# Performance work log

Measured on AMD Instinct MI355X. Metric: run time of the kernel, lower is better.

## Reference

```python
import jax, jax.numpy as jnp
import numpy as np

U, E, V = 1024, 256, 20200

def _w(key, shape):
    fan_in = shape[0] if len(shape) > 1 else shape[0]
    return jax.random.normal(key, shape, dtype=jnp.float32) * (1.0 / np.sqrt(fan_in))

def setup_inputs() -> dict:
    key = jax.random.key(0)
    ks = jax.random.split(key, 20)
    inp = {
        'enc_in': jax.random.randint(ks[0], (32, 64), 0, V),
        'teacher': jax.random.randint(ks[1], (32, 16), 0, V),
        'max_cmd_len': 16,
        'batch_size': 32,
        # encoder params
        'Ee': jax.random.normal(ks[2], (V, E), dtype=jnp.float32) * 0.02,
        'enc_Wx': _w(ks[3], (E, 3 * U)),
        'enc_Wh': _w(ks[4], (U, 3 * U)),
        'enc_b_in': jnp.zeros((3 * U,), jnp.float32),
        'enc_b_rec': jnp.zeros((3 * U,), jnp.float32),
        # decoder params
        'Ed': jax.random.normal(ks[5], (V, E), dtype=jnp.float32) * 0.02,
        'dec_Wx': _w(ks[6], (U + E, 3 * U)),
        'dec_Wh': _w(ks[7], (U, 3 * U)),
        'dec_b_in': jnp.zeros((3 * U,), jnp.float32),
        'dec_b_rec': jnp.zeros((3 * U,), jnp.float32),
        # Bahdanau attention params
        'W1': _w(ks[8], (U, U)), 'b1': jnp.zeros((U,), jnp.float32),
        'W2': _w(ks[9], (U, U)), 'b2': jnp.zeros((U,), jnp.float32),
        'Va': _w(ks[10], (U, 1)), 'bv': jnp.zeros((1,), jnp.float32),
        # output projection
        'Wf': _w(ks[11], (U, V)), 'bf': jnp.zeros((V,), jnp.float32),
    }
    return inp

def gru_step(x, h, Wx, Wh, b_in, b_rec):
    # Keras GRU, reset_after=True, gate order (z, r, h)
    gx = x @ Wx + b_in          # [B, 3U]
    gh = h @ Wh + b_rec         # [B, 3U]
    xz, xr, xh = jnp.split(gx, 3, axis=-1)
    hz, hr, hh = jnp.split(gh, 3, axis=-1)
    z = jax.nn.sigmoid(xz + hz)
    r = jax.nn.sigmoid(xr + hr)
    c = jnp.tanh(xh + r * hh)
    return z * h + (1.0 - z) * c

def reference(enc_in, teacher, max_cmd_len, batch_size,
              Ee, enc_Wx, enc_Wh, enc_b_in, enc_b_rec,
              Ed, dec_Wx, dec_Wh, dec_b_in, dec_b_rec,
              W1, b1, W2, b2, Va, bv, Wf, bf):
    B = enc_in.shape[0]
    # ----- encoder: GRU over source, h0 = 0 -----
    x_emb = Ee[enc_in]                          # [B, S, E]
    def enc_step(h, x_t):
        h_new = gru_step(x_t, h, enc_Wx, enc_Wh, enc_b_in, enc_b_rec)
        return h_new, h_new
    enc_hidden, enc_seq = jax.lax.scan(enc_step, jnp.zeros((B, U), x_emb.dtype),
                                       jnp.swapaxes(x_emb, 0, 1))
    encoded = jnp.swapaxes(enc_seq, 0, 1)       # [B, S, U]

    # ----- decoder: teacher-forced, attention each step -----
    pre_enc = encoded @ W1 + b1                 # precompute W1(encoded): [B, S, U]
    h0_dec = jnp.zeros((B, U), encoded.dtype)   # original calls gru without initial_state

    def dec_step(dec_h, tok):
        q = dec_h @ W2 + b2                                     # [B, U]
        score = jnp.tanh(pre_enc + q[:, None, :]) @ Va + bv     # [B, S, 1]
        attn = jax.nn.softmax(score, axis=1)
        ctx = jnp.sum(attn * encoded, axis=1)                   # [B, U]
        x = jnp.concatenate([ctx, Ed[tok]], axis=-1)            # [B, U+E]
        h_new = gru_step(x, h0_dec, dec_Wx, dec_Wh, dec_b_in, dec_b_rec)
        logits_t = h_new @ Wf + bf                              # [B, V]
        return h_new, logits_t

    toks = jnp.swapaxes(teacher[:, :max_cmd_len], 0, 1)         # [T, B]
    _, logits_tbv = jax.lax.scan(dec_step, enc_hidden, toks)    # [T, B, V]
    logits = jnp.swapaxes(logits_tbv, 0, 1)                     # [B, T, V]
    predictions = jnp.argmax(logits, axis=-1).astype(jnp.int64) # [B, T]
    return logits, predictions
```

## Files before the change

kernel.cpp:

```cpp
#include <hip/hip_runtime.h>
#include <cmath>

#define BB 32
#define SS 64
#define TT 16
#define UU 1024
#define EE 256
#define VV 20200
#define G3 3072
#define NBLK 256

#define WS_XEMBT 0
#define WS_HT    (WS_XEMBT + SS*EE*BB)
#define WS_ENC   (WS_HT + 2*UU*BB)
#define WS_PRE   (WS_ENC + BB*SS*UU)
#define WS_Q     (WS_PRE + BB*SS*UU)
#define WS_ESC   (WS_Q + BB*UU)
#define WS_XT    (WS_ESC + BB*SS)
#define WS_HDT   (WS_XT + UU*BB)
#define WS_HD    (WS_HDT + UU*BB)
#define WS_DEMB  (WS_HD + BB*TT*UU)
#define WS_GXD   (WS_DEMB + BB*TT*EE)
#define WS_BAR   (WS_GXD + BB*TT*G3)

#define ACC4(A, V, S) do { (A).x += (V).x * (S); (A).y += (V).y * (S); \
                           (A).z += (V).z * (S); (A).w += (V).w * (S); } while (0)
#define RED4(A, M) do { (A).x += __shfl_xor((A).x, M, 64); (A).y += __shfl_xor((A).y, M, 64); \
                        (A).z += __shfl_xor((A).z, M, 64); (A).w += __shfl_xor((A).w, M, 64); } while (0)

__device__ __forceinline__ float sigmoidf_(float x) {
    return 1.0f / (1.0f + expf(-x));
}

__device__ __forceinline__ void store_agent(float* p, float v) {
    __hip_atomic_store(p, v, __ATOMIC_RELAXED, __HIP_MEMORY_SCOPE_AGENT);
}
__device__ __forceinline__ void store_agent_u(unsigned* p, unsigned v) {
    __hip_atomic_store(p, v, __ATOMIC_RELAXED, __HIP_MEMORY_SCOPE_AGENT);
}
__device__ __forceinline__ unsigned load_agent_u(unsigned* p) {
    return __hip_atomic_load(p, __ATOMIC_RELAXED, __HIP_MEMORY_SCOPE_AGENT);
}

__device__ __forceinline__ void grid_barrier(unsigned* base, int bid, unsigned g) {
    __syncthreads();
    if (threadIdx.x < 64) {
        const int lane = threadIdx.x;
        const int grp = bid >> 5;
        const unsigned gv = g + 1u;
        if (lane == 0) {
            __builtin_amdgcn_s_waitcnt(0);
            store_agent_u(base + bid, gv);
        }
        if ((bid & 31) == 0) {
            for (;;) {
                unsigned v = load_agent_u(base + grp * 32 + (lane & 31));
                if (__all((int)(v >= gv))) break;
                __builtin_amdgcn_s_sleep(2);
            }
            if (lane == 0) store_agent_u(base + 256 + grp * 32, gv);
            if (bid == 0) {
                for (;;) {
                    unsigned v = load_agent_u(base + 256 + (lane & 7) * 32);
                    if (__all((int)(v >= gv))) break;
                    __builtin_amdgcn_s_sleep(2);
                }
                if (lane < 8) store_agent_u(base + 512 + lane * 32, gv);
            }
        }
        if (bid != 0) {
            while (load_agent_u(base + 512 + grp * 32) < gv) {
                __builtin_amdgcn_s_sleep(2);
            }
        }
        __builtin_amdgcn_fence(__ATOMIC_ACQUIRE, "agent");
    }
    __syncthreads();
}

__global__ __launch_bounds__(256) void k_prep(const int* __restrict__ enc_in,
                                              const float* __restrict__ Ee,
                                              const int* __restrict__ teacher,
                                              const float* __restrict__ Ed,
                                              float* __restrict__ ws) {
    int gid = blockIdx.x * 256 + threadIdx.x;
    const int NE = SS * EE * BB;
    const int NH = UU * BB;
    const int ND = BB * TT * EE;
    if (gid < NE) {
        int b = gid & 31;
        int e = (gid >> 5) & 255;
        int s = gid >> 13;
        ws[WS_XEMBT + gid] = Ee[(size_t)enc_in[b * SS + s] * EE + e];
    } else if (gid < NE + NH) {
        ws[WS_HT + (gid - NE)] = 0.0f;
    } else if (gid < NE + NH + ND) {
        int idx = gid - NE - NH;
        int e = idx & 255;
        int row = idx >> 8;
        int t = row >> 5, b = row & 31;
        ws[WS_DEMB + idx] = Ed[(size_t)teacher[b * TT + t] * EE + e];
    } else if (gid < NE + NH + ND + 3072) {
        ((unsigned*)(ws + WS_BAR))[gid - NE - NH - ND] = 0u;
    }
}

__global__ __launch_bounds__(512, 2) void k_encoder(const float* __restrict__ Wh,
                                                    const float* __restrict__ Wx,
                                                    const float* __restrict__ b_in,
                                                    const float* __restrict__ b_rec,
                                                    float* __restrict__ ws) {
    float* XembT = ws + WS_XEMBT;
    float* hT = ws + WS_HT;
    float* enc = ws + WS_ENC;
    unsigned* bar = (unsigned*)(ws + WS_BAR);

    __shared__ float Whs[12288];
    __shared__ float Wxs[3072];
    __shared__ float scr[4096];

    const int tid = threadIdx.x;
    const int bid = blockIdx.x;
    const int wv = tid >> 6;
    const int lane = tid & 63;
    const int kp = lane & 7;
    const int rg = lane >> 3;

    for (int k = tid; k < 1024; k += 512) {
        #pragma unroll
        for (int g = 0; g < 3; ++g)
            *(float4*)(Whs + k * 12 + g * 4) =
                *(const float4*)(Wh + (size_t)k * G3 + g * 1024 + bid * 4);
    }
    if (tid < 256) {
        int k = tid;
        #pragma unroll
        for (int g = 0; g < 3; ++g)
            *(float4*)(Wxs + k * 12 + g * 4) =
                *(const float4*)(Wx + (size_t)k * G3 + g * 1024 + bid * 4);
    }

    float bz_s = 0.f, br_s = 0.f, bci_s = 0.f, bcr_s = 0.f;
    int rc_ = 0, rb_ = 0, rj_ = 0;
    if (tid < 128) {
        rc_ = tid >> 5; rb_ = tid & 31; rj_ = bid * 4 + rc_;
        bz_s = b_in[rj_] + b_rec[rj_];
        br_s = b_in[1024 + rj_] + b_rec[1024 + rj_];
        bci_s = b_in[2048 + rj_];
        bcr_s = b_rec[2048 + rj_];
    }
    __syncthreads();

    const int hk0 = wv * 128 + kp;
    const int xk0 = wv * 32 + kp;
    float hreg = 0.f;

    for (int t = 0; t < SS; ++t) {
        const float* hprev = hT + (t & 1) * (UU * BB);
        float* hnext = hT + ((t & 1) ^ 1) * (UU * BB);

        float4 az[4], ar[4], ah[4], ax[4];
        #pragma unroll
        for (int c = 0; c < 4; ++c) {
            az[c] = make_float4(0.f, 0.f, 0.f, 0.f);
            ar[c] = make_float4(0.f, 0.f, 0.f, 0.f);
            ah[c] = make_float4(0.f, 0.f, 0.f, 0.f);
            ax[c] = make_float4(0.f, 0.f, 0.f, 0.f);
        }

        {
            const float* hp = hprev + hk0 * 32 + rg * 4;
            float4 hb[16];
            #pragma unroll
            for (int u = 0; u < 16; ++u) hb[u] = *(const float4*)(hp + u * 256);
            #pragma unroll
            for (int u = 0; u < 16; ++u) {
                const float* wp = Whs + (hk0 + 8 * u) * 12;
                float4 wz = *(const float4*)wp;
                float4 wr_ = *(const float4*)(wp + 4);
                float4 wc_ = *(const float4*)(wp + 8);
                float4 hv = hb[u];
                ACC4(az[0], hv, wz.x); ACC4(az[1], hv, wz.y); ACC4(az[2], hv, wz.z); ACC4(az[3], hv, wz.w);
                ACC4(ar[0], hv, wr_.x); ACC4(ar[1], hv, wr_.y); ACC4(ar[2], hv, wr_.z); ACC4(ar[3], hv, wr_.w);
                ACC4(ah[0], hv, wc_.x); ACC4(ah[1], hv, wc_.y); ACC4(ah[2], hv, wc_.z); ACC4(ah[3], hv, wc_.w);
            }
        }
        {
            const float* xp = XembT + t * (EE * BB) + xk0 * 32 + rg * 4;
            float4 xb[4];
            #pragma unroll
            for (int u = 0; u < 4; ++u) xb[u] = *(const float4*)(xp + u * 256);
            #pragma unroll
            for (int u = 0; u < 4; ++u) {
                const float* wp = Wxs + (xk0 + 8 * u) * 12;
                float4 wz = *(const float4*)wp;
                float4 wr_ = *(const float4*)(wp + 4);
                float4 wc_ = *(const float4*)(wp + 8);
                float4 xv = xb[u];
                ACC4(az[0], xv, wz.x); ACC4(az[1], xv, wz.y); ACC4(az[2], xv, wz.z); ACC4(az[3], xv, wz.w);
                ACC4(ar[0], xv, wr_.x); ACC4(ar[1], xv, wr_.y); ACC4(ar[2], xv, wr_.z); ACC4(ar[3], xv, wr_.w);
                ACC4(ax[0], xv, wz.x * 0.f + wc_.x); ACC4(ax[1], xv, wc_.y); ACC4(ax[2], xv, wc_.z); ACC4(ax[3], xv, wc_.w);
            }
        }
        #pragma unroll
        for (int m = 1; m <= 4; m <<= 1) {
            #pragma unroll
            for (int c = 0; c < 4; ++c) { RED4(az[c], m); RED4(ar[c], m); RED4(ah[c], m); RED4(ax[c], m); }
        }
        if (kp == 0) {
            float* sb = scr + wv * 512 + rg * 4;
            #pragma unroll
            for (int c = 0; c < 4; ++c) {
                *(float4*)(sb + c * 32) = az[c];
                *(float4*)(sb + 128 + c * 32) = ar[c];
                *(float4*)(sb + 256 + c * 32) = ah[c];
                *(float4*)(sb + 384 + c * 32) = ax[c];
            }
        }
        __syncthreads();
        if (tid < 128) {
            float saz = 0.f, sar = 0.f, sah = 0.f, sax = 0.f;
            #pragma unroll
            for (int w = 0; w < 8; ++w) {
                const float* sb = scr + w * 512 + rc_ * 32 + rb_;
                saz += sb[0]; sar += sb[128]; sah += sb[256]; sax += sb[384];
            }
            float z = sigmoidf_(saz + bz_s);
            float r = sigmoidf_(sar + br_s);
            float cc = tanhf(sax + bci_s + r * (sah + bcr_s));
            float hnew = z * hreg + (1.0f - z) * cc;
            hreg = hnew;
            store_agent(&hnext[rj_ * 32 + rb_], hnew);
            enc[((size_t)rb_ * SS + t) * UU + rj_] = hnew;
        }
        grid_barrier(bar, bid, (unsigned)t);
    }
}

__global__ __launch_bounds__(256) void k_gemm(const float* __restrict__ A,
                                              const float* __restrict__ Bm,
                                              const float* __restrict__ bias,
                                              float* __restrict__ C,
                                              int M, int N, int K) {
    __shared__ float As[16][68];
    __shared__ float Bs[16][132];
    const int rb = blockIdx.x * 64;
    const int cb = blockIdx.y * 128;
    const int tid = threadIdx.x;
    const int cg = tid & 31;
    const int rg = tid >> 5;
    float acc[8][4] = {{0.f}};

    const int arow = tid >> 2, akq = (tid & 3) * 4;
    const int bkk = tid >> 4, bc8 = (tid & 15) * 8;
    const bool nfull = (cb + 128 <= N);

    for (int k0 = 0; k0 < K; k0 += 16) {
        {
            float4 a4 = *(const float4*)(A + (size_t)(rb + arow) * K + k0 + akq);
            As[akq + 0][arow] = a4.x; As[akq + 1][arow] = a4.y;
            As[akq + 2][arow] = a4.z; As[akq + 3][arow] = a4.w;
        }
        {
            int col = cb + bc8;
            const float* bp = Bm + (size_t)(k0 + bkk) * N + col;
            if (nfull) {
                float4 x0 = *(const float4*)bp;
                float4 x1 = *(const float4*)(bp + 4);
                Bs[bkk][bc8 + 0] = x0.x; Bs[bkk][bc8 + 1] = x0.y; Bs[bkk][bc8 + 2] = x0.z; Bs[bkk][bc8 + 3] = x0.w;
                Bs[bkk][bc8 + 4] = x1.x; Bs[bkk][bc8 + 5] = x1.y; Bs[bkk][bc8 + 6] = x1.z; Bs[bkk][bc8 + 7] = x1.w;
            } else {
                #pragma unroll
                for (int jj = 0; jj < 8; ++jj)
                    Bs[bkk][bc8 + jj] = (col + jj < N) ? bp[jj] : 0.0f;
            }
        }
        __syncthreads();
        #pragma unroll
        for (int kk = 0; kk < 16; ++kk) {
            float4 a0 = *(const float4*)&As[kk][rg * 8];
            float4 a1 = *(const float4*)&As[kk][rg * 8 + 4];
            float4 b0 = *(const float4*)&Bs[kk][cg * 4];
            float av[8] = {a0.x, a0.y, a0.z, a0.w, a1.x, a1.y, a1.z, a1.w};
            float bv[4] = {b0.x, b0.y, b0.z, b0.w};
            #pragma unroll
            for (int i = 0; i < 8; ++i)
                #pragma unroll
                for (int jj = 0; jj < 4; ++jj)
                    acc[i][jj] += av[i] * bv[jj];
        }
        __syncthreads();
    }
    const int col0 = cb + cg * 4;
    const bool cfull = (col0 + 4 <= N);
    #pragma unroll
    for (int i = 0; i < 8; ++i) {
        int row = rb + rg * 8 + i;
        float* cp = C + (size_t)row * N + col0;
        if (cfull) {
            float4 o;
            o.x = acc[i][0] + bias[col0 + 0];
            o.y = acc[i][1] + bias[col0 + 1];
            o.z = acc[i][2] + bias[col0 + 2];
            o.w = acc[i][3] + bias[col0 + 3];
            *(float4*)cp = o;
        } else {
            #pragma unroll
            for (int jj = 0; jj < 4; ++jj)
                if (col0 + jj < N) cp[jj] = acc[i][jj] + bias[col0 + jj];
        }
    }
}

__global__ __launch_bounds__(256) void k_gemm128(const float* __restrict__ A,
                                                 const float* __restrict__ Bm,
                                                 const float* __restrict__ bias,
                                                 float* __restrict__ C,
                                                 int M, int N, int K) {
    __shared__ float As[16][132];
    __shared__ float Bs[16][132];
    const int rb = blockIdx.x * 128;
    const int cb = blockIdx.y * 128;
    const int tid = threadIdx.x;
    const int rg = tid >> 4;
    const int cg = tid & 15;
    float acc[8][8] = {{0.f}};

    const int arow = tid >> 1, akq = (tid & 1) * 8;
    const int bkk = tid >> 4, bc8 = (tid & 15) * 8;
    const bool nfull = (cb + 128 <= N);

    for (int k0 = 0; k0 < K; k0 += 16) {
        {
            const float* ap = A + (size_t)(rb + arow) * K + k0 + akq;
            float4 a0 = *(const float4*)ap;
            float4 a1 = *(const float4*)(ap + 4);
            As[akq + 0][arow] = a0.x; As[akq + 1][arow] = a0.y;
            As[akq + 2][arow] = a0.z; As[akq + 3][arow] = a0.w;
            As[akq + 4][arow] = a1.x; As[akq + 5][arow] = a1.y;
            As[akq + 6][arow] = a1.z; As[akq + 7][arow] = a1.w;
        }
        {
            int col = cb + bc8;
            const float* bp = Bm + (size_t)(k0 + bkk) * N + col;
            if (nfull) {
                *(float4*)&Bs[bkk][bc8] = *(const float4*)bp;
                *(float4*)&Bs[bkk][bc8 + 4] = *(const float4*)(bp + 4);
            } else {
                #pragma unroll
                for (int jj = 0; jj < 8; ++jj)
                    Bs[bkk][bc8 + jj] = (col + jj < N) ? bp[jj] : 0.0f;
            }
        }
        __syncthreads();
        #pragma unroll
        for (int kk = 0; kk < 16; ++kk) {
            float4 a0 = *(const float4*)&As[kk][rg * 8];
            float4 a1 = *(const float4*)&As[kk][rg * 8 + 4];
            float4 b0 = *(const float4*)&Bs[kk][cg * 8];
            float4 b1 = *(const float4*)&Bs[kk][cg * 8 + 4];
            float av[8] = {a0.x, a0.y, a0.z, a0.w, a1.x, a1.y, a1.z, a1.w};
            float bw[8] = {b0.x, b0.y, b0.z, b0.w, b1.x, b1.y, b1.z, b1.w};
            #pragma unroll
            for (int i = 0; i < 8; ++i)
                #pragma unroll
                for (int jj = 0; jj < 8; ++jj)
                    acc[i][jj] += av[i] * bw[jj];
        }
        __syncthreads();
    }
    const int col0 = cb + cg * 8;
    const bool cfull = (col0 + 8 <= N);
    #pragma unroll
    for (int i = 0; i < 8; ++i) {
        int row = rb + rg * 8 + i;
        float* cp = C + (size_t)row * N + col0;
        if (cfull) {
            float4 o0, o1;
            o0.x = acc[i][0] + bias[col0 + 0];
            o0.y = acc[i][1] + bias[col0 + 1];
            o0.z = acc[i][2] + bias[col0 + 2];
            o0.w = acc[i][3] + bias[col0 + 3];
            o1.x = acc[i][4] + bias[col0 + 4];
            o1.y = acc[i][5] + bias[col0 + 5];
            o1.z = acc[i][6] + bias[col0 + 6];
            o1.w = acc[i][7] + bias[col0 + 7];
            *(float4*)cp = o0;
            *(float4*)(cp + 4) = o1;
        } else {
            #pragma unroll
            for (int jj = 0; jj < 8; ++jj)
                if (col0 + jj < N) cp[jj] = acc[i][jj] + bias[col0 + jj];
        }
    }
}

__global__ __launch_bounds__(256, 1) void k_decoder(const float* __restrict__ W2,
                                                    const float* __restrict__ b2,
                                                    const float* __restrict__ Va,
                                                    const float* __restrict__ bv,
                                                    const float* __restrict__ Wxd,
                                                    const float* __restrict__ b_rec,
                                                    float* __restrict__ ws) {
    float* hT = ws + WS_HT;
    float* enc = ws + WS_ENC;
    float* pre = ws + WS_PRE;
    float* q = ws + WS_Q;
    float* esc = ws + WS_ESC;
    float* xT = ws + WS_XT;
    float* hdT = ws + WS_HDT;
    float* Hd = ws + WS_HD;
    float* GXd = ws + WS_GXD;
    unsigned* bar = (unsigned*)(ws + WS_BAR) + 1024;

    __shared__ float Wxds[12288];
    __shared__ float W2s[4096];
    __shared__ float scr[1536];
    __shared__ float eL[64];
    __shared__ float attnL[64];
    __shared__ float shs[256];

    const int tid = threadIdx.x;
    const int bid = blockIdx.x;
    const int wv = tid >> 6;
    const int lane = tid & 63;
    const int kp = lane & 7;
    const int rg = lane >> 3;

    for (int k = tid; k < 1024; k += 256) {
        #pragma unroll
        for (int g = 0; g < 3; ++g)
            *(float4*)(Wxds + k * 12 + g * 4) =
                *(const float4*)(Wxd + (size_t)k * G3 + g * 1024 + bid * 4);
        *(float4*)(W2s + k * 4) = *(const float4*)(W2 + (size_t)k * UU + bid * 4);
    }

    float bzr_s = 0.f, brr_s = 0.f, bcr_s = 0.f;
    int rc_ = 0, rb_ = 0, rj_ = 0;
    if (tid < 128) {
        rc_ = tid >> 5; rb_ = tid & 31; rj_ = bid * 4 + rc_;
        bzr_s = b_rec[rj_];
        brr_s = b_rec[1024 + rj_];
        bcr_s = b_rec[2048 + rj_];
    }
    __syncthreads();

    const int xk0 = wv * 256 + kp;
    unsigned bc = 0;

    for (int t = 0; t < TT; ++t) {
        const float* hsrc = (t == 0) ? hT : hdT;

        float gxz = 0.f, gxr = 0.f, gxc = 0.f;
        if (tid < 128) {
            const float* gx = GXd + (size_t)(t * BB + rb_) * G3;
            gxz = gx[rj_];
            gxr = gx[1024 + rj_];
            gxc = gx[2048 + rj_];
        }

        {
            const int cq = lane & 3;
            const int kpq = (lane >> 2) & 7;
            const int rgq = (lane >> 5) | (wv << 1);
            const int qc = bid * 4 + cq;
            const float* hp = hsrc + kpq * 32 + rgq * 4;
            float a0 = 0, a1 = 0, a2 = 0, a3 = 0;
            for (int g = 0; g < 16; ++g) {
                float4 hv[8]; float wr[8];
                #pragma unroll
                for (int u = 0; u < 8; ++u) {
                    hv[u] = *(const float4*)(hp + (g * 8 + u) * 256);
                    wr[u] = W2s[(kpq + 8 * (g * 8 + u)) * 4 + cq];
                }
                #pragma unroll
                for (int u = 0; u < 8; ++u) {
                    a0 += hv[u].x * wr[u]; a1 += hv[u].y * wr[u];
                    a2 += hv[u].z * wr[u]; a3 += hv[u].w * wr[u];
                }
            }
            #pragma unroll
            for (int m = 4; m <= 16; m <<= 1) {
                a0 += __shfl_xor(a0, m, 64); a1 += __shfl_xor(a1, m, 64);
                a2 += __shfl_xor(a2, m, 64); a3 += __shfl_xor(a3, m, 64);
            }
            if (kpq == 0) {
                float bb2 = b2[qc];
                store_agent(&q[(size_t)(rgq * 4 + 0) * UU + qc], a0 + bb2);
                store_agent(&q[(size_t)(rgq * 4 + 1) * UU + qc], a1 + bb2);
                store_agent(&q[(size_t)(rgq * 4 + 2) * UU + qc], a2 + bb2);
                store_agent(&q[(size_t)(rgq * 4 + 3) * UU + qc], a3 + bb2);
            }
        }
        grid_barrier(bar, bid, bc++);

        {
            const int b = bid >> 3, s0 = (bid & 7) * 8;
            const int pi = tid >> 5, kq = tid & 31;
            const int srow = s0 + pi;
            const float* pe = pre + ((size_t)b * SS + srow) * UU;
            const float* qb = q + (size_t)b * UU;
            float acc = 0;
            #pragma unroll
            for (int kk = 0; kk < 8; ++kk) {
                int k = kq * 32 + kk * 4;
                float4 p4 = *(const float4*)(pe + k);
                float4 q4 = *(const float4*)(qb + k);
                float4 v4 = *(const float4*)(Va + k);
                acc += tanhf(p4.x + q4.x) * v4.x + tanhf(p4.y + q4.y) * v4.y +
                       tanhf(p4.z + q4.z) * v4.z + tanhf(p4.w + q4.w) * v4.w;
            }
            #pragma unroll
            for (int m = 16; m >= 1; m >>= 1) acc += __shfl_xor(acc, m, 32);
            if (kq == 0) store_agent(&esc[b * SS + srow], acc + bv[0]);
        }
        grid_barrier(bar, bid, bc++);

        {
            const int b = bid >> 3, ug = bid & 7;
            if (tid < 64) eL[tid] = esc[b * SS + tid];
            __syncthreads();
            if (tid < 64) {
                float v = eL[tid];
                float m = v;
                #pragma unroll
                for (int mm = 32; mm >= 1; mm >>= 1) m = fmaxf(m, __shfl_xor(m, mm, 64));
                float p = expf(v - m);
                float sum = p;
                #pragma unroll
                for (int mm = 32; mm >= 1; mm >>= 1) sum += __shfl_xor(sum, mm, 64);
                attnL[tid] = p / sum;
            }
            __syncthreads();
            const int u = ug * 128 + (tid & 127), sp = tid >> 7;
            float acc = 0;
            #pragma unroll 8
            for (int i = 0; i < 32; ++i) {
                int srow = sp * 32 + i;
                acc += attnL[srow] * enc[((size_t)b * SS + srow) * UU + u];
            }
            shs[(tid & 127) * 2 + sp] = acc;
            __syncthreads();
            if (tid < 128)
                store_agent(&xT[(size_t)(ug * 128 + tid) * BB + b], shs[tid * 2] + shs[tid * 2 + 1]);
        }
        grid_barrier(bar, bid, bc++);

        {
            float4 sz[4], sr_[4], sc_[4];
            #pragma unroll
            for (int c = 0; c < 4; ++c) {
                sz[c] = make_float4(0.f, 0.f, 0.f, 0.f);
                sr_[c] = make_float4(0.f, 0.f, 0.f, 0.f);
                sc_[c] = make_float4(0.f, 0.f, 0.f, 0.f);
            }
            const float* xp = xT + xk0 * 32 + rg * 4;
            #pragma unroll
            for (int gg = 0; gg < 2; ++gg) {
                float4 xb[16];
                #pragma unroll
                for (int u = 0; u < 16; ++u) xb[u] = *(const float4*)(xp + (gg * 16 + u) * 256);
                #pragma unroll
                for (int u = 0; u < 16; ++u) {
                    const float* wp = Wxds + (xk0 + 8 * (gg * 16 + u)) * 12;
                    float4 wz = *(const float4*)wp;
                    float4 wr4 = *(const float4*)(wp + 4);
                    float4 wc4 = *(const float4*)(wp + 8);
                    float4 xv = xb[u];
                    ACC4(sz[0], xv, wz.x); ACC4(sz[1], xv, wz.y); ACC4(sz[2], xv, wz.z); ACC4(sz[3], xv, wz.w);
                    ACC4(sr_[0], xv, wr4.x); ACC4(sr_[1], xv, wr4.y); ACC4(sr_[2], xv, wr4.z); ACC4(sr_[3], xv, wr4.w);
                    ACC4(sc_[0], xv, wc4.x); ACC4(sc_[1], xv, wc4.y); ACC4(sc_[2], xv, wc4.z); ACC4(sc_[3], xv, wc4.w);
                }
            }
            #pragma unroll
            for (int m = 1; m <= 4; m <<= 1) {
                #pragma unroll
                for (int c = 0; c < 4; ++c) { RED4(sz[c], m); RED4(sr_[c], m); RED4(sc_[c], m); }
            }
            if (kp == 0) {
                float* sb = scr + wv * 384 + rg * 4;
                #pragma unroll
                for (int c = 0; c < 4; ++c) {
                    *(float4*)(sb + c * 32) = sz[c];
                    *(float4*)(sb + 128 + c * 32) = sr_[c];
                    *(float4*)(sb + 256 + c * 32) = sc_[c];
                }
            }
            __syncthreads();
            if (tid < 128) {
                float ssz = 0.f, ssr = 0.f, ssc = 0.f;
                #pragma unroll
                for (int w = 0; w < 4; ++w) {
                    const float* sb = scr + w * 384 + rc_ * 32 + rb_;
                    ssz += sb[0]; ssr += sb[128]; ssc += sb[256];
                }
                float z = sigmoidf_(ssz + gxz + bzr_s);
                float rr = sigmoidf_(ssr + gxr + brr_s);
                float cc = tanhf(ssc + gxc + rr * bcr_s);
                float h = (1.0f - z) * cc;
                Hd[((size_t)rb_ * TT + t) * UU + rj_] = h;
                store_agent(&hdT[(size_t)rj_ * BB + rb_], h);
            }
        }
        grid_barrier(bar, bid, bc++);
    }
}

__global__ __launch_bounds__(256) void k_argmax(const float* __restrict__ logits,
                                                float* __restrict__ outp) {
    const int row = blockIdx.x;
    const float* lr = logits + (size_t)row * VV;
    const int tid = threadIdx.x;
    float best = -INFINITY;
    int bidx = 0x7fffffff;
    for (int c = tid; c < VV; c += 256) {
        float v = lr[c];
        if (v > best) { best = v; bidx = c; }
    }
    __shared__ float bv_[256];
    __shared__ int bi_[256];
    bv_[tid] = best; bi_[tid] = bidx;
    __syncthreads();
    for (int s2 = 128; s2 > 0; s2 >>= 1) {
        if (tid < s2) {
            float ov = bv_[tid + s2]; int oi = bi_[tid + s2];
            if (ov > bv_[tid] || (ov == bv_[tid] && oi < bi_[tid])) {
                bv_[tid] = ov; bi_[tid] = oi;
            }
        }
        __syncthreads();
    }
    if (tid == 0) outp[row] = (float)bi_[0];
}

extern "C" void kernel_launch(void* const* d_in, const int* in_sizes, int n_in,
                              void* d_out, int out_size, void* d_ws, size_t ws_size,
                              hipStream_t stream) {
    const int* enc_in = (const int*)d_in[0];
    const int* teacher = (const int*)d_in[1];
    const float* Ee = (const float*)d_in[4];
    const float* eWx = (const float*)d_in[5];
    const float* eWh = (const float*)d_in[6];
    const float* eb_in = (const float*)d_in[7];
    const float* eb_rec = (const float*)d_in[8];
    const float* Ed = (const float*)d_in[9];
    const float* dWx = (const float*)d_in[10];
    const float* db_in = (const float*)d_in[12];
    const float* db_rec = (const float*)d_in[13];
    const float* W1 = (const float*)d_in[14];
    const float* b1 = (const float*)d_in[15];
    const float* W2 = (const float*)d_in[16];
    const float* b2 = (const float*)d_in[17];
    const float* Va = (const float*)d_in[18];
    const float* bvv = (const float*)d_in[19];
    const float* Wf = (const float*)d_in[20];
    const float* bf = (const float*)d_in[21];
    float* ws = (float*)d_ws;
    float* out = (float*)d_out;

    const int NTOT = SS * EE * BB + UU * BB + BB * TT * EE + 3072;
    k_prep<<<dim3((NTOT + 255) / 256), dim3(256), 0, stream>>>(enc_in, Ee, teacher, Ed, ws);

    k_gemm<<<dim3(8, 24), dim3(256), 0, stream>>>(ws + WS_DEMB, dWx + (size_t)UU * G3, db_in,
                                                  ws + WS_GXD, BB * TT, G3, EE);

    k_encoder<<<dim3(NBLK), dim3(512), 0, stream>>>(eWh, eWx, eb_in, eb_rec, ws);

    k_gemm<<<dim3(32, 8), dim3(256), 0, stream>>>(ws + WS_ENC, W1, b1, ws + WS_PRE, BB * SS, UU, UU);

    k_decoder<<<dim3(NBLK), dim3(256), 0, stream>>>(W2, b2, Va, bvv, dWx, db_rec, ws);

    k_gemm128<<<dim3(4, 158), dim3(256), 0, stream>>>(ws + WS_HD, Wf, bf, out, BB * TT, VV, UU);

    k_argmax<<<dim3(BB * TT), dim3(256), 0, stream>>>(out, out + (size_t)BB * TT * VV);
}
```

Measured before the change: 2.098 ms.

## Use cache-bypassing loads for cross-block data, drop barrier acquire fence, widen decoder

Replaces the agent-scope acquire fence in the grid barrier with explicit sc0 sc1 global loads for data written by other blocks (hidden state, q, scores, context), so only those reads bypass non-coherent caches. The decoder grows to 512 threads per block, which halves each thread's K-slice for the W2 query, attention score and GRU input products and adds an LDS cross-wave reduction for q. In the encoder the recurrent h load is moved after the input projection. The goal is lower per-step latency in the barrier-bound recurrent loops. The risk is memory-ordering bugs from removing the fence, plus more register pressure and LDS use.

```diff
diff --git a/kernel.cpp b/kernel.cpp
--- a/kernel.cpp
+++ b/kernel.cpp
@@ -28,6 +28,8 @@
 #define RED4(A, M) do { (A).x += __shfl_xor((A).x, M, 64); (A).y += __shfl_xor((A).y, M, 64); \
                         (A).z += __shfl_xor((A).z, M, 64); (A).w += __shfl_xor((A).w, M, 64); } while (0)
 
+typedef float f4v __attribute__((ext_vector_type(4)));
+
 __device__ __forceinline__ float sigmoidf_(float x) {
     return 1.0f / (1.0f + expf(-x));
 }
@@ -40,6 +42,51 @@
 }
 __device__ __forceinline__ unsigned load_agent_u(unsigned* p) {
     return __hip_atomic_load(p, __ATOMIC_RELAXED, __HIP_MEMORY_SCOPE_AGENT);
+}
+
+__device__ __forceinline__ void llc_load16(const float* p, f4v* o) {
+    asm volatile(
+        "global_load_dwordx4 %0, %16, off sc0 sc1\n\t"
+        "global_load_dwordx4 %1, %16, off offset:1024 sc0 sc1\n\t"
+        "global_load_dwordx4 %2, %16, off offset:2048 sc0 sc1\n\t"
+        "global_load_dwordx4 %3, %16, off offset:3072 sc0 sc1\n\t"
+        "global_load_dwordx4 %4, %17, off sc0 sc1\n\t"
+        "global_load_dwordx4 %5, %17, off offset:1024 sc0 sc1\n\t"
+        "global_load_dwordx4 %6, %17, off offset:2048 sc0 sc1\n\t"
+        "global_load_dwordx4 %7, %17, off offset:3072 sc0 sc1\n\t"
+        "global_load_dwordx4 %8, %18, off sc0 sc1\n\t"
+        "global_load_dwordx4 %9, %18, off offset:1024 sc0 sc1\n\t"
+        "global_load_dwordx4 %10, %18, off offset:2048 sc0 sc1\n\t"
+        "global_load_dwordx4 %11, %18, off offset:3072 sc0 sc1\n\t"
+        "global_load_dwordx4 %12, %19, off sc0 sc1\n\t"
+        "global_load_dwordx4 %13, %19, off offset:1024 sc0 sc1\n\t"
+        "global_load_dwordx4 %14, %19, off offset:2048 sc0 sc1\n\t"
+        "global_load_dwordx4 %15, %19, off offset:3072 sc0 sc1\n\t"
+        "s_waitcnt vmcnt(0)"
+        : "=&v"(o[0]), "=&v"(o[1]), "=&v"(o[2]), "=&v"(o[3]),
+          "=&v"(o[4]), "=&v"(o[5]), "=&v"(o[6]), "=&v"(o[7]),
+          "=&v"(o[8]), "=&v"(o[9]), "=&v"(o[10]), "=&v"(o[11]),
+          "=&v"(o[12]), "=&v"(o[13]), "=&v"(o[14]), "=&v"(o[15])
+        : "v"(p), "v"(p + 1024), "v"(p + 2048), "v"(p + 3072)
+        : "memory");
+}
+
+__device__ __forceinline__ void llc_load4(const float* p, f4v* o) {
+    asm volatile(
+        "global_load_dwordx4 %0, %4, off sc0 sc1\n\t"
+        "global_load_dwordx4 %1, %4, off offset:16 sc0 sc1\n\t"
+        "global_load_dwordx4 %2, %4, off offset:32 sc0 sc1\n\t"
+        "global_load_dwordx4 %3, %4, off offset:48 sc0 sc1\n\t"
+        "s_waitcnt vmcnt(0)"
+        : "=&v"(o[0]), "=&v"(o[1]), "=&v"(o[2]), "=&v"(o[3])
+        : "v"(p) : "memory");
+}
+
+__device__ __forceinline__ float llc_loadf(const float* p) {
+    float r;
+    asm volatile("global_load_dword %0, %1, off sc0 sc1\n\ts_waitcnt vmcnt(0)"
+                 : "=&v"(r) : "v"(p) : "memory");
+    return r;
 }
 
 __device__ __forceinline__ void grid_barrier(unsigned* base, int bid, unsigned g) {
@@ -49,6 +96,7 @@
         const int grp = bid >> 5;
         const unsigned gv = g + 1u;
         if (lane == 0) {
+            asm volatile("" ::: "memory");
             __builtin_amdgcn_s_waitcnt(0);
             store_agent_u(base + bid, gv);
         }
@@ -73,7 +121,6 @@
                 __builtin_amdgcn_s_sleep(2);
             }
         }
-        __builtin_amdgcn_fence(__ATOMIC_ACQUIRE, "agent");
     }
     __syncthreads();
 }
@@ -169,23 +216,6 @@
         }
 
         {
-            const float* hp = hprev + hk0 * 32 + rg * 4;
-            float4 hb[16];
-            #pragma unroll
-            for (int u = 0; u < 16; ++u) hb[u] = *(const float4*)(hp + u * 256);
-            #pragma unroll
-            for (int u = 0; u < 16; ++u) {
-                const float* wp = Whs + (hk0 + 8 * u) * 12;
-                float4 wz = *(const float4*)wp;
-                float4 wr_ = *(const float4*)(wp + 4);
-                float4 wc_ = *(const float4*)(wp + 8);
-                float4 hv = hb[u];
-                ACC4(az[0], hv, wz.x); ACC4(az[1], hv, wz.y); ACC4(az[2], hv, wz.z); ACC4(az[3], hv, wz.w);
-                ACC4(ar[0], hv, wr_.x); ACC4(ar[1], hv, wr_.y); ACC4(ar[2], hv, wr_.z); ACC4(ar[3], hv, wr_.w);
-                ACC4(ah[0], hv, wc_.x); ACC4(ah[1], hv, wc_.y); ACC4(ah[2], hv, wc_.z); ACC4(ah[3], hv, wc_.w);
-            }
-        }
-        {
             const float* xp = XembT + t * (EE * BB) + xk0 * 32 + rg * 4;
             float4 xb[4];
             #pragma unroll
@@ -199,7 +229,22 @@
                 float4 xv = xb[u];
                 ACC4(az[0], xv, wz.x); ACC4(az[1], xv, wz.y); ACC4(az[2], xv, wz.z); ACC4(az[3], xv, wz.w);
                 ACC4(ar[0], xv, wr_.x); ACC4(ar[1], xv, wr_.y); ACC4(ar[2], xv, wr_.z); ACC4(ar[3], xv, wr_.w);
-                ACC4(ax[0], xv, wz.x * 0.f + wc_.x); ACC4(ax[1], xv, wc_.y); ACC4(ax[2], xv, wc_.z); ACC4(ax[3], xv, wc_.w);
+                ACC4(ax[0], xv, wc_.x); ACC4(ax[1], xv, wc_.y); ACC4(ax[2], xv, wc_.z); ACC4(ax[3], xv, wc_.w);
+            }
+        }
+        {
+            f4v hb[16];
+            llc_load16(hprev + hk0 * 32 + rg * 4, hb);
+            #pragma unroll
+            for (int u = 0; u < 16; ++u) {
+                const float* wp = Whs + (hk0 + 8 * u) * 12;
+                float4 wz = *(const float4*)wp;
+                float4 wr_ = *(const float4*)(wp + 4);
+                float4 wc_ = *(const float4*)(wp + 8);
+                f4v hv = hb[u];
+                ACC4(az[0], hv, wz.x); ACC4(az[1], hv, wz.y); ACC4(az[2], hv, wz.z); ACC4(az[3], hv, wz.w);
+                ACC4(ar[0], hv, wr_.x); ACC4(ar[1], hv, wr_.y); ACC4(ar[2], hv, wr_.z); ACC4(ar[3], hv, wr_.w);
+                ACC4(ah[0], hv, wc_.x); ACC4(ah[1], hv, wc_.y); ACC4(ah[2], hv, wc_.z); ACC4(ah[3], hv, wc_.w);
             }
         }
         #pragma unroll
@@ -395,7 +440,7 @@
     }
 }
 
-__global__ __launch_bounds__(256, 1) void k_decoder(const float* __restrict__ W2,
+__global__ __launch_bounds__(512, 2) void k_decoder(const float* __restrict__ W2,
                                                     const float* __restrict__ b2,
                                                     const float* __restrict__ Va,
                                                     const float* __restrict__ bv,
@@ -415,10 +460,10 @@
 
     __shared__ float Wxds[12288];
     __shared__ float W2s[4096];
-    __shared__ float scr[1536];
+    __shared__ float scr[3072];
     __shared__ float eL[64];
     __shared__ float attnL[64];
-    __shared__ float shs[256];
+    __shared__ float shs[512];
 
     const int tid = threadIdx.x;
     const int bid = blockIdx.x;
@@ -427,7 +472,7 @@
     const int kp = lane & 7;
     const int rg = lane >> 3;
 
-    for (int k = tid; k < 1024; k += 256) {
+    for (int k = tid; k < 1024; k += 512) {
         #pragma unroll
         for (int g = 0; g < 3; ++g)
             *(float4*)(Wxds + k * 12 + g * 4) =
@@ -435,17 +480,18 @@
         *(float4*)(W2s + k * 4) = *(const float4*)(W2 + (size_t)k * UU + bid * 4);
     }
 
-    float bzr_s = 0.f, brr_s = 0.f, bcr_s = 0.f;
+    float bzr_s = 0.f, brr_s = 0.f, bcr_s = 0.f, b2s = 0.f;
     int rc_ = 0, rb_ = 0, rj_ = 0;
     if (tid < 128) {
         rc_ = tid >> 5; rb_ = tid & 31; rj_ = bid * 4 + rc_;
         bzr_s = b_rec[rj_];
         brr_s = b_rec[1024 + rj_];
         bcr_s = b_rec[2048 + rj_];
+        b2s = b2[rj_];
     }
     __syncthreads();
 
-    const int xk0 = wv * 256 + kp;
+    const int hk0 = wv * 128 + kp;
     unsigned bc = 0;
 
     for (int t = 0; t < TT; ++t) {
@@ -460,65 +506,65 @@
         }
 
         {
-            const int cq = lane & 3;
-            const int kpq = (lane >> 2) & 7;
-            const int rgq = (lane >> 5) | (wv << 1);
-            const int qc = bid * 4 + cq;
-            const float* hp = hsrc + kpq * 32 + rgq * 4;
-            float a0 = 0, a1 = 0, a2 = 0, a3 = 0;
-            for (int g = 0; g < 16; ++g) {
-                float4 hv[8]; float wr[8];
-                #pragma unroll
-                for (int u = 0; u < 8; ++u) {
-                    hv[u] = *(const float4*)(hp + (g * 8 + u) * 256);
-                    wr[u] = W2s[(kpq + 8 * (g * 8 + u)) * 4 + cq];
-                }
-                #pragma unroll
-                for (int u = 0; u < 8; ++u) {
-                    a0 += hv[u].x * wr[u]; a1 += hv[u].y * wr[u];
-                    a2 += hv[u].z * wr[u]; a3 += hv[u].w * wr[u];
-                }
-            }
-            #pragma unroll
-            for (int m = 4; m <= 16; m <<= 1) {
-                a0 += __shfl_xor(a0, m, 64); a1 += __shfl_xor(a1, m, 64);
-                a2 += __shfl_xor(a2, m, 64); a3 += __shfl_xor(a3, m, 64);
-            }
-            if (kpq == 0) {
-                float bb2 = b2[qc];
-                store_agent(&q[(size_t)(rgq * 4 + 0) * UU + qc], a0 + bb2);
-                store_agent(&q[(size_t)(rgq * 4 + 1) * UU + qc], a1 + bb2);
-                store_agent(&q[(size_t)(rgq * 4 + 2) * UU + qc], a2 + bb2);
-                store_agent(&q[(size_t)(rgq * 4 + 3) * UU + qc], a3 + bb2);
+            f4v hb[16];
+            llc_load16(hsrc + hk0 * 32 + rg * 4, hb);
+            float4 aq[4];
+            #pragma unroll
+            for (int c = 0; c < 4; ++c) aq[c] = make_float4(0.f, 0.f, 0.f, 0.f);
+            #pragma unroll
+            for (int u = 0; u < 16; ++u) {
+                f4v w4 = *(const f4v*)(W2s + (hk0 + 8 * u) * 4);
+                f4v hv = hb[u];
+                ACC4(aq[0], hv, w4.x); ACC4(aq[1], hv, w4.y);
+                ACC4(aq[2], hv, w4.z); ACC4(aq[3], hv, w4.w);
+            }
+            #pragma unroll
+            for (int m = 1; m <= 4; m <<= 1) {
+                #pragma unroll
+                for (int c = 0; c < 4; ++c) RED4(aq[c], m);
+            }
+            if (kp == 0) {
+                float* sb = scr + wv * 128 + rg * 4;
+                #pragma unroll
+                for (int c = 0; c < 4; ++c) *(float4*)(sb + c * 32) = aq[c];
+            }
+            __syncthreads();
+            if (tid < 128) {
+                float s = 0.f;
+                #pragma unroll
+                for (int w = 0; w < 8; ++w) s += scr[w * 128 + rc_ * 32 + rb_];
+                store_agent(&q[(size_t)rb_ * UU + rj_], s + b2s);
             }
         }
         grid_barrier(bar, bid, bc++);
 
         {
             const int b = bid >> 3, s0 = (bid & 7) * 8;
-            const int pi = tid >> 5, kq = tid & 31;
+            const int pi = tid >> 6;
+            const int kq = lane;
             const int srow = s0 + pi;
-            const float* pe = pre + ((size_t)b * SS + srow) * UU;
-            const float* qb = q + (size_t)b * UU;
+            const float* pe = pre + ((size_t)b * SS + srow) * UU + kq * 16;
+            const float* va = Va + kq * 16;
+            f4v q4[4];
+            llc_load4(q + (size_t)b * UU + kq * 16, q4);
             float acc = 0;
             #pragma unroll
-            for (int kk = 0; kk < 8; ++kk) {
-                int k = kq * 32 + kk * 4;
-                float4 p4 = *(const float4*)(pe + k);
-                float4 q4 = *(const float4*)(qb + k);
-                float4 v4 = *(const float4*)(Va + k);
-                acc += tanhf(p4.x + q4.x) * v4.x + tanhf(p4.y + q4.y) * v4.y +
-                       tanhf(p4.z + q4.z) * v4.z + tanhf(p4.w + q4.w) * v4.w;
-            }
-            #pragma unroll
-            for (int m = 16; m >= 1; m >>= 1) acc += __shfl_xor(acc, m, 32);
+            for (int kk = 0; kk < 4; ++kk) {
+                float4 p4 = *(const float4*)(pe + kk * 4);
+                float4 v4 = *(const float4*)(va + kk * 4);
+                f4v qq = q4[kk];
+                acc += tanhf(p4.x + qq.x) * v4.x + tanhf(p4.y + qq.y) * v4.y +
+                       tanhf(p4.z + qq.z) * v4.z + tanhf(p4.w + qq.w) * v4.w;
+            }
+            #pragma unroll
+            for (int m = 1; m <= 32; m <<= 1) acc += __shfl_xor(acc, m, 64);
             if (kq == 0) store_agent(&esc[b * SS + srow], acc + bv[0]);
         }
         grid_barrier(bar, bid, bc++);
 
         {
             const int b = bid >> 3, ug = bid & 7;
-            if (tid < 64) eL[tid] = esc[b * SS + tid];
+            if (tid < 64) eL[tid] = llc_loadf(&esc[b * SS + tid]);
             __syncthreads();
             if (tid < 64) {
                 float v = eL[tid];
@@ -535,14 +581,15 @@
             const int u = ug * 128 + (tid & 127), sp = tid >> 7;
             float acc = 0;
             #pragma unroll 8
-            for (int i = 0; i < 32; ++i) {
-                int srow = sp * 32 + i;
+            for (int i = 0; i < 16; ++i) {
+                int srow = sp * 16 + i;
                 acc += attnL[srow] * enc[((size_t)b * SS + srow) * UU + u];
             }
-            shs[(tid & 127) * 2 + sp] = acc;
+            shs[(tid & 127) * 4 + sp] = acc;
             __syncthreads();
             if (tid < 128)
-                store_agent(&xT[(size_t)(ug * 128 + tid) * BB + b], shs[tid * 2] + shs[tid * 2 + 1]);
+                store_agent(&xT[(size_t)(ug * 128 + tid) * BB + b],
+                            shs[tid * 4] + shs[tid * 4 + 1] + shs[tid * 4 + 2] + shs[tid * 4 + 3]);
         }
         grid_barrier(bar, bid, bc++);
 
@@ -554,23 +601,18 @@
                 sr_[c] = make_float4(0.f, 0.f, 0.f, 0.f);
                 sc_[c] = make_float4(0.f, 0.f, 0.f, 0.f);
             }
-            const float* xp = xT + xk0 * 32 + rg * 4;
-            #pragma unroll
-            for (int gg = 0; gg < 2; ++gg) {
-                float4 xb[16];
-                #pragma unroll
-                for (int u = 0; u < 16; ++u) xb[u] = *(const float4*)(xp + (gg * 16 + u) * 256);
-                #pragma unroll
-                for (int u = 0; u < 16; ++u) {
-                    const float* wp = Wxds + (xk0 + 8 * (gg * 16 + u)) * 12;
-                    float4 wz = *(const float4*)wp;
-                    float4 wr4 = *(const float4*)(wp + 4);
-                    float4 wc4 = *(const float4*)(wp + 8);
-                    float4 xv = xb[u];
-                    ACC4(sz[0], xv, wz.x); ACC4(sz[1], xv, wz.y); ACC4(sz[2], xv, wz.z); ACC4(sz[3], xv, wz.w);
-                    ACC4(sr_[0], xv, wr4.x); ACC4(sr_[1], xv, wr4.y); ACC4(sr_[2], xv, wr4.z); ACC4(sr_[3], xv, wr4.w);
-                    ACC4(sc_[0], xv, wc4.x); ACC4(sc_[1], xv, wc4.y); ACC4(sc_[2], xv, wc4.z); ACC4(sc_[3], xv, wc4.w);
-                }
+            f4v xb[16];
+            llc_load16(xT + hk0 * 32 + rg * 4, xb);
+            #pragma unroll
+            for (int u = 0; u < 16; ++u) {
+                const float* wp = Wxds + (hk0 + 8 * u) * 12;
+                float4 wz = *(const float4*)wp;
+                float4 wr4 = *(const float4*)(wp + 4);
+                float4 wc4 = *(const float4*)(wp + 8);
+                f4v xv = xb[u];
+                ACC4(sz[0], xv, wz.x); ACC4(sz[1], xv, wz.y); ACC4(sz[2], xv, wz.z); ACC4(sz[3], xv, wz.w);
+                ACC4(sr_[0], xv, wr4.x); ACC4(sr_[1], xv, wr4.y); ACC4(sr_[2], xv, wr4.z); ACC4(sr_[3], xv, wr4.w);
+                ACC4(sc_[0], xv, wc4.x); ACC4(sc_[1], xv, wc4.y); ACC4(sc_[2], xv, wc4.z); ACC4(sc_[3], xv, wc4.w);
             }
             #pragma unroll
             for (int m = 1; m <= 4; m <<= 1) {
@@ -590,7 +632,7 @@
             if (tid < 128) {
                 float ssz = 0.f, ssr = 0.f, ssc = 0.f;
                 #pragma unroll
-                for (int w = 0; w < 4; ++w) {
+                for (int w = 0; w < 8; ++w) {
                     const float* sb = scr + w * 384 + rc_ * 32 + rb_;
                     ssz += sb[0]; ssr += sb[128]; ssc += sb[256];
                 }
@@ -668,7 +710,7 @@
 
     k_gemm<<<dim3(32, 8), dim3(256), 0, stream>>>(ws + WS_ENC, W1, b1, ws + WS_PRE, BB * SS, UU, UU);
 
-    k_decoder<<<dim3(NBLK), dim3(256), 0, stream>>>(W2, b2, Va, bvv, dWx, db_rec, ws);
+    k_decoder<<<dim3(NBLK), dim3(512), 0, stream>>>(W2, b2, Va, bvv, dWx, db_rec, ws);
 
     k_gemm128<<<dim3(4, 158), dim3(256), 0, stream>>>(ws + WS_HD, Wf, bf, out, BB * TT, VV, UU);
 
```

After: 1.919 ms. 8.5% less time.
